# Kernel optimization log

Measured on AMD Instinct MI355X. Metric: run time of the kernel, lower is better.

## Reference

```python
import jax, jax.numpy as jnp
import numpy as np

NUM_HEADS = 16
NUM_T = 8
L1D = 16  # img_size // patch_size


def _freqs_1d(dim, end, base=10000.0):
    f = 1.0 / (base ** (jnp.arange(0, dim, 2, dtype=jnp.float32) / dim))  # [dim/2]
    ang = jnp.outer(jnp.arange(end, dtype=jnp.float32), f)                # [end, dim/2]
    return jnp.cos(ang), jnp.sin(ang)


def _freqs_2d(dim, h, w, base=10000.0):
    f = 1.0 / (base ** (jnp.arange(0, dim, 4, dtype=jnp.float32)[: dim // 4] / dim))  # [dim/4]
    ax = jnp.outer(jnp.arange(w, dtype=jnp.float32), f)  # [w, dim/4]
    ay = jnp.outer(jnp.arange(h, dtype=jnp.float32), f)  # [h, dim/4]
    # flatten order: position index = y*w + x
    ang_x = jnp.broadcast_to(ax[None, :, :], (h, w, dim // 4)).reshape(h * w, dim // 4)
    ang_y = jnp.broadcast_to(ay[:, None, :], (h, w, dim // 4)).reshape(h * w, dim // 4)
    ang = jnp.concatenate([ang_x, ang_y], axis=-1)  # [h*w, dim/2]
    return jnp.cos(ang), jnp.sin(ang)


def _rope(x, cos, sin):
    # x: [..., P, d]; cos/sin: [P, d/2]; interleaved complex pairs (x0,x1),(x2,x3),...
    xr, xi = x[..., 0::2], x[..., 1::2]
    or_ = xr * cos - xi * sin
    oi = xr * sin + xi * cos
    return jnp.stack([or_, oi], axis=-1).reshape(x.shape)


def setup_inputs() -> dict:
    key = jax.random.key(0)
    ks = jax.random.split(key, 5)
    H = 1024
    return {
        "x": jax.random.normal(ks[0], (2, 2048, H), dtype=jnp.float32),
        "w_qkv": jax.random.normal(ks[1], (3 * H, H), dtype=jnp.float32) * 0.02,
        "b_qkv": jax.random.normal(ks[2], (3 * H,), dtype=jnp.float32) * 0.02,
        "w_out": jax.random.normal(ks[3], (H, H), dtype=jnp.float32) * 0.02,
        "b_out": jax.random.normal(ks[4], (H,), dtype=jnp.float32) * 0.02,
    }


def reference(x, w_qkv, b_qkv, w_out, b_out):
    B, L, H = x.shape
    n, t = NUM_HEADS, NUM_T
    hd = H // n
    Ls = L // t  # spatial tokens per frame (= L1D*L1D)

    # QKV projection; per-head layout [q|k|v] of size 3*hd (matches torch rearrange+chunk)
    qkv = (x @ w_qkv.T + b_qkv).reshape(B, L, n, 3 * hd)
    q, k, v = qkv[..., :hd], qkv[..., hd:2 * hd], qkv[..., 2 * hd:]

    cos_s, sin_s = _freqs_2d(hd, L1D, L1D)  # [Ls, hd/2]
    cos_t, sin_t = _freqs_1d(hd, t)         # [t, hd/2]

    def to_bntl(a):  # (B, L=t*Ls, n, hd) -> (B, n, t, Ls, hd)
        return a.reshape(B, t, Ls, n, hd).transpose(0, 3, 1, 2, 4)

    q = _rope(to_bntl(q), cos_s, sin_s)
    k = _rope(to_bntl(k), cos_s, sin_s)
    # temporal rope: rotate over t axis
    q = _rope(q.transpose(0, 1, 3, 2, 4), cos_t, sin_t).transpose(0, 1, 3, 2, 4)
    k = _rope(k.transpose(0, 1, 3, 2, 4), cos_t, sin_t).transpose(0, 1, 3, 2, 4)
    q = q.reshape(B, n, L, hd)
    k = k.reshape(B, n, L, hd)
    v = v.transpose(0, 2, 1, 3)  # (B, n, L, hd)

    scores = jnp.einsum('bnqd,bnkd->bnqk', q, k) / jnp.sqrt(jnp.asarray(hd, jnp.float32))
    idx = jnp.arange(L)
    neg = jnp.finfo(jnp.float32).min
    causal = jnp.where(idx[None, :] <= idx[:, None], 0.0, neg)  # [L, L]
    attn = jax.nn.softmax((scores + causal).astype(jnp.float32), axis=-1).astype(x.dtype)

    o = jnp.einsum('bnqk,bnkd->bnqd', attn, v).transpose(0, 2, 1, 3).reshape(B, L, H)
    o = o * jax.nn.sigmoid(o)  # swish
    return o @ w_out.T + b_out
```

## Files before the change

kernel.cpp:

```cpp
#include <hip/hip_runtime.h>
#include <math.h>

#define B_SZ 2
#define L_SEQ 2048
#define H_SZ 1024
#define NH 16
#define HD 64
#define QSCALE 0.18033688011112042f

typedef __attribute__((ext_vector_type(8))) short frag_ab;
typedef __attribute__((ext_vector_type(4))) float frag_cd;
typedef __attribute__((ext_vector_type(8))) unsigned short u16x8;
typedef __attribute__((ext_vector_type(4))) unsigned short u16x4;

__device__ __forceinline__ unsigned short f2bf(float f) {
  unsigned int x = __builtin_bit_cast(unsigned int, f);
  x += 0x7fffu + ((x >> 16) & 1u);
  return (unsigned short)(x >> 16);
}
__device__ __forceinline__ float bf2f(unsigned int u) {
  return __builtin_bit_cast(float, u << 16);
}
__device__ __forceinline__ unsigned int cvt_pk_bf16(float lo, float hi) {
  unsigned int r;
  asm("v_cvt_pk_bf16_f32 %0, %1, %2" : "=v"(r) : "v"(lo), "v"(hi));
  return r;
}
__device__ __forceinline__ void gload16(const void* g, void* l) {
  __builtin_amdgcn_global_load_lds((const __attribute__((address_space(1))) void*)g,
                                   (__attribute__((address_space(3))) void*)l, 16, 0, 0);
}

__device__ __forceinline__ void cvt8(const float* __restrict__ in,
                                     unsigned short* __restrict__ out, int i) {
  float4 a = *(const float4*)&in[i];
  float4 b = *(const float4*)&in[i + 4];
  u16x8 o = {f2bf(a.x), f2bf(a.y), f2bf(a.z), f2bf(a.w),
             f2bf(b.x), f2bf(b.y), f2bf(b.z), f2bf(b.w)};
  *(u16x8*)&out[i] = o;
}

__global__ __launch_bounds__(256) void glue_pre_k(
    const float* __restrict__ x, const float* __restrict__ wq, const float* __restrict__ wo,
    unsigned short* __restrict__ xb, unsigned short* __restrict__ wqb,
    unsigned short* __restrict__ wob, float2* __restrict__ ctab) {
  int bx = blockIdx.x, tid = threadIdx.x;
  if (bx < 256) {
    int idx = bx * 256 + tid;
    int l = idx >> 5, j = idx & 31;
    int ti = l >> 8;
    int s = l & 255;
    float ang_s;
    if (j < 16) ang_s = (float)(s & 15) * powf(10000.f, -(float)j / 16.f);
    else        ang_s = (float)(s >> 4) * powf(10000.f, -(float)(j - 16) / 16.f);
    float ang_t = (float)ti * powf(10000.f, -(float)j / 32.f);
    float a = ang_s + ang_t;
    ctab[idx] = make_float2(cosf(a), sinf(a));
  } else if (bx < 2304) {
    cvt8(x, xb, ((bx - 256) * 256 + tid) * 8);
  } else if (bx < 3840) {
    cvt8(wq, wqb, ((bx - 2304) * 256 + tid) * 8);
  } else {
    cvt8(wo, wob, ((bx - 3840) * 256 + tid) * 8);
  }
}

#define G_ISSUE(k0, bi)                                                        \
  _Pragma("unroll") for (int it = 0; it < 2; ++it) {                           \
    int c = tid + it * 256;                                                    \
    int row = c >> 2, e0 = (c & 3) * 8;                                        \
    gload16(A + (size_t)(m0 + row) * K + (k0) + e0, &As[bi][c * 8]);           \
    gload16(W + (size_t)(n0 + row) * K + (k0) + e0, &Ws[bi][c * 8]);           \
  }

__global__ __launch_bounds__(256) void gemm_qkv_fused_k(
    const unsigned short* __restrict__ A, const unsigned short* __restrict__ W,
    const float* __restrict__ bias, const float2* __restrict__ ctab,
    unsigned short* __restrict__ Qb, unsigned short* __restrict__ Kb,
    unsigned short* __restrict__ Vt) {
  const int K = 1024, N = 3072;
  __shared__ unsigned short As[2][128 * 32];
  __shared__ unsigned short Ws[2][128 * 32];
  const frag_cd fzero = {0.f, 0.f, 0.f, 0.f};
  int tid = threadIdx.x;
  int nbx = N >> 7;
  int nwg = gridDim.x;
  int bid = blockIdx.x;
  int qq = nwg >> 3;
  int bidx = (bid & 7) * qq + (bid >> 3);
  int m0 = (bidx / nbx) * 128, n0 = (bidx % nbx) * 128;
  int w = tid >> 6, lane = tid & 63, t = lane & 15, g = lane >> 4;
  int wm = w >> 1, wn = w & 1;
  frag_cd acc[4][4];
#pragma unroll
  for (int mi = 0; mi < 4; ++mi)
#pragma unroll
    for (int ni = 0; ni < 4; ++ni) acc[mi][ni] = fzero;

  G_ISSUE(0, 0);
  __syncthreads();
  int kb = 0;
  for (int k0 = 0; k0 < K; k0 += 32, kb ^= 1) {
    if (k0 + 32 < K) { G_ISSUE(k0 + 32, kb ^ 1); }
    frag_ab af[4], wf[4];
#pragma unroll
    for (int mi = 0; mi < 4; ++mi)
      af[mi] = *(const frag_ab*)&As[kb][(wm * 64 + mi * 16 + t) * 32 + 8 * g];
#pragma unroll
    for (int ni = 0; ni < 4; ++ni)
      wf[ni] = *(const frag_ab*)&Ws[kb][(wn * 64 + ni * 16 + t) * 32 + 8 * g];
    __builtin_amdgcn_s_setprio(1);
#pragma unroll
    for (int mi = 0; mi < 4; ++mi)
#pragma unroll
      for (int ni = 0; ni < 4; ++ni)
        acc[mi][ni] = __builtin_amdgcn_mfma_f32_16x16x32_bf16(af[mi], wf[ni], acc[mi][ni], 0, 0, 0);
    __builtin_amdgcn_s_setprio(0);
    __syncthreads();
  }

#pragma unroll
  for (int ni = 0; ni < 4; ++ni) {
    int cb = n0 + wn * 64 + ni * 16;
    int region = (cb >> 6) % 3;
    int head = cb / 192;
    int d = (cb & 63) + t;
    float bv = bias[cb + t];
    if (region == 2) {
#pragma unroll
      for (int mi = 0; mi < 4; ++mi) {
        int row0 = m0 + wm * 64 + mi * 16 + g * 4;
        int bb = row0 >> 11, l0 = row0 & 2047;
        u16x4 ov;
#pragma unroll
        for (int r = 0; r < 4; ++r) ov[r] = f2bf(acc[mi][ni][r] + bv);
        *(u16x4*)&Vt[((size_t)((bb * NH + head) * HD + d)) * L_SEQ + l0] = ov;
      }
    } else {
      float qs = (region == 0) ? QSCALE : 1.f;
      float sgn = (t & 1) ? qs : -qs;
      unsigned short* dst = (region == 0) ? Qb : Kb;
      int j = d >> 1;
#pragma unroll
      for (int mi = 0; mi < 4; ++mi) {
        int row0 = m0 + wm * 64 + mi * 16 + g * 4;
        int bb = row0 >> 11, l0 = row0 & 2047;
        size_t obase = ((size_t)(bb * NH + head) * L_SEQ + l0) * HD + d;
#pragma unroll
        for (int r = 0; r < 4; ++r) {
          float v = acc[mi][ni][r] + bv;
          float p = __shfl_xor(v, 1);
          float2 cs = ctab[(l0 + r) * 32 + j];
          float o = v * (cs.x * qs) + p * (cs.y * sgn);
          dst[obase + (size_t)r * HD] = f2bf(o);
        }
      }
    }
  }
}

__global__ __launch_bounds__(256) void gemm_mfma_k(
    const unsigned short* __restrict__ A, const unsigned short* __restrict__ W,
    const float* __restrict__ bias, float* __restrict__ C, int M, int N, int K) {
  __shared__ unsigned short As[2][128 * 32];
  __shared__ unsigned short Ws[2][128 * 32];
  const frag_cd fzero = {0.f, 0.f, 0.f, 0.f};
  int tid = threadIdx.x;
  int nbx = N >> 7;
  int nwg = gridDim.x;
  int bid = blockIdx.x;
  int qq = nwg >> 3;
  int bidx = (bid & 7) * qq + (bid >> 3);
  int m0 = (bidx / nbx) * 128, n0 = (bidx % nbx) * 128;
  int w = tid >> 6, lane = tid & 63, t = lane & 15, g = lane >> 4;
  int wm = w >> 1, wn = w & 1;
  frag_cd acc[4][4];
#pragma unroll
  for (int mi = 0; mi < 4; ++mi)
#pragma unroll
    for (int ni = 0; ni < 4; ++ni) acc[mi][ni] = fzero;

  G_ISSUE(0, 0);
  __syncthreads();
  int kb = 0;
  for (int k0 = 0; k0 < K; k0 += 32, kb ^= 1) {
    if (k0 + 32 < K) { G_ISSUE(k0 + 32, kb ^ 1); }
    frag_ab af[4], wf[4];
#pragma unroll
    for (int mi = 0; mi < 4; ++mi)
      af[mi] = *(const frag_ab*)&As[kb][(wm * 64 + mi * 16 + t) * 32 + 8 * g];
#pragma unroll
    for (int ni = 0; ni < 4; ++ni)
      wf[ni] = *(const frag_ab*)&Ws[kb][(wn * 64 + ni * 16 + t) * 32 + 8 * g];
    __builtin_amdgcn_s_setprio(1);
#pragma unroll
    for (int mi = 0; mi < 4; ++mi)
#pragma unroll
      for (int ni = 0; ni < 4; ++ni)
        acc[mi][ni] = __builtin_amdgcn_mfma_f32_16x16x32_bf16(af[mi], wf[ni], acc[mi][ni], 0, 0, 0);
    __builtin_amdgcn_s_setprio(0);
    __syncthreads();
  }
#pragma unroll
  for (int mi = 0; mi < 4; ++mi)
#pragma unroll
    for (int ni = 0; ni < 4; ++ni) {
      int col = n0 + wn * 64 + ni * 16 + t;
      float bv = bias[col];
#pragma unroll
      for (int r = 0; r < 4; ++r)
        C[(size_t)(m0 + wm * 64 + mi * 16 + g * 4 + r) * N + col] = acc[mi][ni][r] + bv;
    }
}

__device__ __forceinline__ void attn_tile(
    const unsigned short* __restrict__ Ksb, const unsigned short* __restrict__ Vsb,
    unsigned short* __restrict__ pw,
    const frag_ab* qf, frag_cd* oacc, float& l_run,
    int qrow, bool diag, int kt, int t, int g) {
  const frag_cd cinit = {-32.f, -32.f, -32.f, -32.f};
  frag_cd st[4];
  __builtin_amdgcn_s_setprio(1);
#pragma unroll
  for (int kb = 0; kb < 4; ++kb) {
    frag_ab k0f = *(const frag_ab*)&Ksb[(((kb * 16 + t) * 64) + 8 * g) ^ ((t & 7) << 3)];
    frag_ab k1f = *(const frag_ab*)&Ksb[(((kb * 16 + t) * 64) + 32 + 8 * g) ^ ((t & 7) << 3)];
    st[kb] = __builtin_amdgcn_mfma_f32_16x16x32_bf16(k0f, qf[0], cinit, 0, 0, 0);
    st[kb] = __builtin_amdgcn_mfma_f32_16x16x32_bf16(k1f, qf[1], st[kb], 0, 0, 0);
  }
  __builtin_amdgcn_s_setprio(0);
  float sv[16];
#pragma unroll
  for (int kb = 0; kb < 4; ++kb)
#pragma unroll
    for (int r = 0; r < 4; ++r) {
      float x = st[kb][r];
      if (diag && (kt * 64 + kb * 16 + g * 4 + r) > qrow) x = -1e30f;
      sv[kb * 4 + r] = x;
    }
  float psum = 0.f;
  unsigned int pk[8];
#pragma unroll
  for (int i = 0; i < 8; ++i) {
    float p0 = __builtin_amdgcn_exp2f(sv[2 * i]);
    float p1 = __builtin_amdgcn_exp2f(sv[2 * i + 1]);
    psum += p0 + p1;
    pk[i] = cvt_pk_bf16(p0, p1);
  }
  psum += __shfl_xor(psum, 16);
  psum += __shfl_xor(psum, 32);
  l_run += psum;

#pragma unroll
  for (int kb = 0; kb < 4; ++kb) {
    uint2 pr = {pk[kb * 2], pk[kb * 2 + 1]};
    *(uint2*)&pw[(t * 64 + kb * 16 + g * 4) ^ ((t & 7) << 3)] = pr;
  }
  frag_ab pf0 = *(const frag_ab*)&pw[(t * 64 + 8 * g) ^ ((t & 7) << 3)];
  frag_ab pf1 = *(const frag_ab*)&pw[(t * 64 + 32 + 8 * g) ^ ((t & 7) << 3)];
  const frag_cd fzero = {0.f, 0.f, 0.f, 0.f};
  (void)fzero;
  __builtin_amdgcn_s_setprio(1);
#pragma unroll
  for (int db = 0; db < 4; ++db) {
    frag_ab v0f = *(const frag_ab*)&Vsb[(((db * 16 + t) * 64) + 8 * g) ^ ((t & 7) << 3)];
    frag_ab v1f = *(const frag_ab*)&Vsb[(((db * 16 + t) * 64) + 32 + 8 * g) ^ ((t & 7) << 3)];
    oacc[db] = __builtin_amdgcn_mfma_f32_16x16x32_bf16(v0f, pf0, oacc[db], 0, 0, 0);
    oacc[db] = __builtin_amdgcn_mfma_f32_16x16x32_bf16(v1f, pf1, oacc[db], 0, 0, 0);
  }
  __builtin_amdgcn_s_setprio(0);
}

__global__ __launch_bounds__(512) void attn_mfma_k(
    const unsigned short* __restrict__ Qg, const unsigned short* __restrict__ Kg,
    const unsigned short* __restrict__ Vt, unsigned short* __restrict__ Og) {
  __shared__ unsigned short Ks[2][64 * 64];
  __shared__ unsigned short Vs[2][64 * 64];
  __shared__ unsigned short Ps[8][16 * 64];
  const frag_cd fzero = {0.f, 0.f, 0.f, 0.f};
  int bx = blockIdx.x;
  int qtA = bx & 15;
  int n = (bx >> 4) & 15;
  int b = bx >> 8;
  int qtB = 31 - qtA;
  int tid = threadIdx.x;
  int w = tid >> 6, lane = tid & 63, t = lane & 15, g = lane >> 4;
  int side = w >> 2;
  int qt = side ? qtA : qtB;
  size_t kvbase = ((size_t)(b * NH + n)) * L_SEQ * HD;
  int qrow = qt * 64 + (w & 3) * 16 + t;

  const unsigned short* qp = Qg + kvbase + (size_t)qrow * HD;
  frag_ab qf[2] = {*(const frag_ab*)(qp + 8 * g), *(const frag_ab*)(qp + 32 + 8 * g)};

  frag_cd oacc[4];
#pragma unroll
  for (int db = 0; db < 4; ++db) oacc[db] = fzero;
  float l_run = 0.f;

  int srow = tid >> 3, se0 = (tid & 7) * 8;
  int sdst = (srow * 64 + se0) ^ ((srow & 7) << 3);
  u16x8 kreg = *(const u16x8*)(Kg + kvbase + (size_t)srow * HD + se0);
  u16x8 vreg = *(const u16x8*)(Vt + kvbase + (size_t)srow * L_SEQ + se0);
  *(u16x8*)&Ks[0][sdst] = kreg;
  *(u16x8*)&Vs[0][sdst] = vreg;

  for (int kt = 0; kt <= qtB; ++kt) {
    int cur = kt & 1;
    __syncthreads();
    if (kt < qtB) {
      kreg = *(const u16x8*)(Kg + kvbase + (size_t)((kt + 1) * 64 + srow) * HD + se0);
      vreg = *(const u16x8*)(Vt + kvbase + (size_t)srow * L_SEQ + (kt + 1) * 64 + se0);
    }
    if (kt <= qt)
      attn_tile(&Ks[cur][0], &Vs[cur][0], &Ps[w][0], qf, oacc, l_run, qrow,
                kt == qt, kt, t, g);
    if (kt < qtB) {
      int nxt = cur ^ 1;
      *(u16x8*)&Ks[nxt][sdst] = kreg;
      *(u16x8*)&Vs[nxt][sdst] = vreg;
    }
  }

  size_t ob0 = (size_t)b * L_SEQ * H_SZ + n * 64;
  float inv = 1.f / l_run;
#pragma unroll
  for (int db = 0; db < 4; ++db) {
    u16x4 ov;
#pragma unroll
    for (int r = 0; r < 4; ++r) {
      float o = oacc[db][r] * inv;
      o = o / (1.f + __expf(-o));
      ov[r] = f2bf(o);
    }
    *(u16x4*)&Og[ob0 + (size_t)qrow * H_SZ + db * 16 + g * 4] = ov;
  }
}

extern "C" void kernel_launch(void* const* d_in, const int* in_sizes, int n_in,
                              void* d_out, int out_size, void* d_ws, size_t ws_size,
                              hipStream_t stream) {
  const float* x = (const float*)d_in[0];
  const float* w_qkv = (const float*)d_in[1];
  const float* b_qkv = (const float*)d_in[2];
  const float* w_out = (const float*)d_in[3];
  const float* b_out = (const float*)d_in[4];
  float* out = (float*)d_out;

  float* ws = (float*)d_ws;
  float2* ctab = (float2*)ws;
  unsigned short* us = (unsigned short*)(ws + 131072);
  unsigned short* Qb = us;
  unsigned short* Kb = Qb + 4194304;
  unsigned short* Vt = Kb + 4194304;
  unsigned short* Og = Vt + 4194304;
  unsigned short* xb = Og + 4194304;
  unsigned short* wqkvb = xb + 4194304;
  unsigned short* woutb = wqkvb + 3145728;

  glue_pre_k<<<4352, 256, 0, stream>>>(x, w_qkv, w_out, xb, wqkvb, woutb, ctab);

  gemm_qkv_fused_k<<<768, 256, 0, stream>>>(xb, wqkvb, b_qkv, ctab, Qb, Kb, Vt);

  attn_mfma_k<<<B_SZ * NH * 16, 512, 0, stream>>>(Qb, Kb, Vt, Og);

  gemm_mfma_k<<<256, 256, 0, stream>>>(Og, woutb, b_out, out, 4096, 1024, 1024);
}
```

Before: 113.1 us.

## Transpose rope table and Q layout, halve out-GEMM M tile, defer softmax row sum

The rope cos/sin table is stored j-major, so the QKV epilogue reads four consecutive positions with two vector loads instead of four scattered float2 loads. Q is now written transposed (d-major, like V), so each write is a 4-wide vector store; the attention kernel in turn gathers Q fragments with strided scalar loads. The output projection GEMM uses a 64x128 tile and launches 512 blocks instead of 256, which fills more CUs at the cost of less reuse per block. The softmax denominator is kept per lane and reduced across lanes only once at the end, removing two shuffles per key tile.

```diff
diff --git a/kernel.cpp b/kernel.cpp
--- a/kernel.cpp
+++ b/kernel.cpp
@@ -47,7 +47,7 @@
   int bx = blockIdx.x, tid = threadIdx.x;
   if (bx < 256) {
     int idx = bx * 256 + tid;
-    int l = idx >> 5, j = idx & 31;
+    int j = idx >> 11, l = idx & 2047;
     int ti = l >> 8;
     int s = l & 255;
     float ang_s;
@@ -76,7 +76,7 @@
 __global__ __launch_bounds__(256) void gemm_qkv_fused_k(
     const unsigned short* __restrict__ A, const unsigned short* __restrict__ W,
     const float* __restrict__ bias, const float2* __restrict__ ctab,
-    unsigned short* __restrict__ Qb, unsigned short* __restrict__ Kb,
+    unsigned short* __restrict__ Qt, unsigned short* __restrict__ Kb,
     unsigned short* __restrict__ Vt) {
   const int K = 1024, N = 3072;
   __shared__ unsigned short As[2][128 * 32];
@@ -136,33 +136,57 @@
         for (int r = 0; r < 4; ++r) ov[r] = f2bf(acc[mi][ni][r] + bv);
         *(u16x4*)&Vt[((size_t)((bb * NH + head) * HD + d)) * L_SEQ + l0] = ov;
       }
+    } else if (region == 0) {
+      float sgn = (t & 1) ? QSCALE : -QSCALE;
+      int j = d >> 1;
+#pragma unroll
+      for (int mi = 0; mi < 4; ++mi) {
+        int row0 = m0 + wm * 64 + mi * 16 + g * 4;
+        int bb = row0 >> 11, l0 = row0 & 2047;
+        const float2* cp = ctab + (size_t)j * 2048 + l0;
+        float4 v01 = *(const float4*)cp;
+        float4 v23 = *(const float4*)(cp + 2);
+        float cvec[4] = {v01.x, v01.z, v23.x, v23.z};
+        float svec[4] = {v01.y, v01.w, v23.y, v23.w};
+        u16x4 ov;
+#pragma unroll
+        for (int r = 0; r < 4; ++r) {
+          float v = acc[mi][ni][r] + bv;
+          float p = __shfl_xor(v, 1);
+          float o = v * (cvec[r] * QSCALE) + p * (svec[r] * sgn);
+          ov[r] = f2bf(o);
+        }
+        *(u16x4*)&Qt[((size_t)((bb * NH + head) * HD + d)) * L_SEQ + l0] = ov;
+      }
     } else {
-      float qs = (region == 0) ? QSCALE : 1.f;
-      float sgn = (t & 1) ? qs : -qs;
-      unsigned short* dst = (region == 0) ? Qb : Kb;
+      float sgn = (t & 1) ? 1.f : -1.f;
       int j = d >> 1;
 #pragma unroll
       for (int mi = 0; mi < 4; ++mi) {
         int row0 = m0 + wm * 64 + mi * 16 + g * 4;
         int bb = row0 >> 11, l0 = row0 & 2047;
         size_t obase = ((size_t)(bb * NH + head) * L_SEQ + l0) * HD + d;
+        const float2* cp = ctab + (size_t)j * 2048 + l0;
+        float4 v01 = *(const float4*)cp;
+        float4 v23 = *(const float4*)(cp + 2);
+        float cvec[4] = {v01.x, v01.z, v23.x, v23.z};
+        float svec[4] = {v01.y, v01.w, v23.y, v23.w};
 #pragma unroll
         for (int r = 0; r < 4; ++r) {
           float v = acc[mi][ni][r] + bv;
           float p = __shfl_xor(v, 1);
-          float2 cs = ctab[(l0 + r) * 32 + j];
-          float o = v * (cs.x * qs) + p * (cs.y * sgn);
-          dst[obase + (size_t)r * HD] = f2bf(o);
+          float o = v * cvec[r] + p * (svec[r] * sgn);
+          Kb[obase + (size_t)r * HD] = f2bf(o);
         }
       }
     }
   }
 }
 
-__global__ __launch_bounds__(256) void gemm_mfma_k(
+__global__ __launch_bounds__(256) void gemm_out_k(
     const unsigned short* __restrict__ A, const unsigned short* __restrict__ W,
     const float* __restrict__ bias, float* __restrict__ C, int M, int N, int K) {
-  __shared__ unsigned short As[2][128 * 32];
+  __shared__ unsigned short As[2][64 * 32];
   __shared__ unsigned short Ws[2][128 * 32];
   const frag_cd fzero = {0.f, 0.f, 0.f, 0.f};
   int tid = threadIdx.x;
@@ -171,30 +195,41 @@
   int bid = blockIdx.x;
   int qq = nwg >> 3;
   int bidx = (bid & 7) * qq + (bid >> 3);
-  int m0 = (bidx / nbx) * 128, n0 = (bidx % nbx) * 128;
+  int m0 = (bidx / nbx) * 64, n0 = (bidx % nbx) * 128;
   int w = tid >> 6, lane = tid & 63, t = lane & 15, g = lane >> 4;
   int wm = w >> 1, wn = w & 1;
-  frag_cd acc[4][4];
-#pragma unroll
-  for (int mi = 0; mi < 4; ++mi)
+  frag_cd acc[2][4];
+#pragma unroll
+  for (int mi = 0; mi < 2; ++mi)
 #pragma unroll
     for (int ni = 0; ni < 4; ++ni) acc[mi][ni] = fzero;
 
-  G_ISSUE(0, 0);
+#define G_ISSUE2(k0, bi)                                                       \
+  {                                                                            \
+    int rowA = tid >> 2, e0A = (tid & 3) * 8;                                  \
+    gload16(A + (size_t)(m0 + rowA) * K + (k0) + e0A, &As[bi][tid * 8]);       \
+    _Pragma("unroll") for (int it = 0; it < 2; ++it) {                         \
+      int c = tid + it * 256;                                                  \
+      int row = c >> 2, e0 = (c & 3) * 8;                                      \
+      gload16(W + (size_t)(n0 + row) * K + (k0) + e0, &Ws[bi][c * 8]);         \
+    }                                                                          \
+  }
+
+  G_ISSUE2(0, 0);
   __syncthreads();
   int kb = 0;
   for (int k0 = 0; k0 < K; k0 += 32, kb ^= 1) {
-    if (k0 + 32 < K) { G_ISSUE(k0 + 32, kb ^ 1); }
-    frag_ab af[4], wf[4];
-#pragma unroll
-    for (int mi = 0; mi < 4; ++mi)
-      af[mi] = *(const frag_ab*)&As[kb][(wm * 64 + mi * 16 + t) * 32 + 8 * g];
+    if (k0 + 32 < K) { G_ISSUE2(k0 + 32, kb ^ 1); }
+    frag_ab af[2], wf[4];
+#pragma unroll
+    for (int mi = 0; mi < 2; ++mi)
+      af[mi] = *(const frag_ab*)&As[kb][(wm * 32 + mi * 16 + t) * 32 + 8 * g];
 #pragma unroll
     for (int ni = 0; ni < 4; ++ni)
       wf[ni] = *(const frag_ab*)&Ws[kb][(wn * 64 + ni * 16 + t) * 32 + 8 * g];
     __builtin_amdgcn_s_setprio(1);
 #pragma unroll
-    for (int mi = 0; mi < 4; ++mi)
+    for (int mi = 0; mi < 2; ++mi)
 #pragma unroll
       for (int ni = 0; ni < 4; ++ni)
         acc[mi][ni] = __builtin_amdgcn_mfma_f32_16x16x32_bf16(af[mi], wf[ni], acc[mi][ni], 0, 0, 0);
@@ -202,21 +237,21 @@
     __syncthreads();
   }
 #pragma unroll
-  for (int mi = 0; mi < 4; ++mi)
+  for (int mi = 0; mi < 2; ++mi)
 #pragma unroll
     for (int ni = 0; ni < 4; ++ni) {
       int col = n0 + wn * 64 + ni * 16 + t;
       float bv = bias[col];
 #pragma unroll
       for (int r = 0; r < 4; ++r)
-        C[(size_t)(m0 + wm * 64 + mi * 16 + g * 4 + r) * N + col] = acc[mi][ni][r] + bv;
+        C[(size_t)(m0 + wm * 32 + mi * 16 + g * 4 + r) * N + col] = acc[mi][ni][r] + bv;
     }
 }
 
 __device__ __forceinline__ void attn_tile(
     const unsigned short* __restrict__ Ksb, const unsigned short* __restrict__ Vsb,
     unsigned short* __restrict__ pw,
-    const frag_ab* qf, frag_cd* oacc, float& l_run,
+    const frag_ab* qf, frag_cd* oacc, float& l_part,
     int qrow, bool diag, int kt, int t, int g) {
   const frag_cd cinit = {-32.f, -32.f, -32.f, -32.f};
   frag_cd st[4];
@@ -229,27 +264,20 @@
     st[kb] = __builtin_amdgcn_mfma_f32_16x16x32_bf16(k1f, qf[1], st[kb], 0, 0, 0);
   }
   __builtin_amdgcn_s_setprio(0);
-  float sv[16];
-#pragma unroll
-  for (int kb = 0; kb < 4; ++kb)
-#pragma unroll
-    for (int r = 0; r < 4; ++r) {
-      float x = st[kb][r];
-      if (diag && (kt * 64 + kb * 16 + g * 4 + r) > qrow) x = -1e30f;
-      sv[kb * 4 + r] = x;
-    }
-  float psum = 0.f;
   unsigned int pk[8];
 #pragma unroll
   for (int i = 0; i < 8; ++i) {
-    float p0 = __builtin_amdgcn_exp2f(sv[2 * i]);
-    float p1 = __builtin_amdgcn_exp2f(sv[2 * i + 1]);
-    psum += p0 + p1;
+    int kb = i >> 1, r0 = (2 * i) & 3;
+    float x0 = st[kb][r0], x1 = st[kb][r0 + 1];
+    if (diag) {
+      if ((kt * 64 + kb * 16 + g * 4 + r0) > qrow) x0 = -1e30f;
+      if ((kt * 64 + kb * 16 + g * 4 + r0 + 1) > qrow) x1 = -1e30f;
+    }
+    float p0 = __builtin_amdgcn_exp2f(x0);
+    float p1 = __builtin_amdgcn_exp2f(x1);
+    l_part += p0 + p1;
     pk[i] = cvt_pk_bf16(p0, p1);
   }
-  psum += __shfl_xor(psum, 16);
-  psum += __shfl_xor(psum, 32);
-  l_run += psum;
 
 #pragma unroll
   for (int kb = 0; kb < 4; ++kb) {
@@ -258,8 +286,6 @@
   }
   frag_ab pf0 = *(const frag_ab*)&pw[(t * 64 + 8 * g) ^ ((t & 7) << 3)];
   frag_ab pf1 = *(const frag_ab*)&pw[(t * 64 + 32 + 8 * g) ^ ((t & 7) << 3)];
-  const frag_cd fzero = {0.f, 0.f, 0.f, 0.f};
-  (void)fzero;
   __builtin_amdgcn_s_setprio(1);
 #pragma unroll
   for (int db = 0; db < 4; ++db) {
@@ -272,7 +298,7 @@
 }
 
 __global__ __launch_bounds__(512) void attn_mfma_k(
-    const unsigned short* __restrict__ Qg, const unsigned short* __restrict__ Kg,
+    const unsigned short* __restrict__ Qt, const unsigned short* __restrict__ Kg,
     const unsigned short* __restrict__ Vt, unsigned short* __restrict__ Og) {
   __shared__ unsigned short Ks[2][64 * 64];
   __shared__ unsigned short Vs[2][64 * 64];
@@ -290,13 +316,19 @@
   size_t kvbase = ((size_t)(b * NH + n)) * L_SEQ * HD;
   int qrow = qt * 64 + (w & 3) * 16 + t;
 
-  const unsigned short* qp = Qg + kvbase + (size_t)qrow * HD;
-  frag_ab qf[2] = {*(const frag_ab*)(qp + 8 * g), *(const frag_ab*)(qp + 32 + 8 * g)};
+  const unsigned short* qtp = Qt + kvbase + qrow;
+  frag_ab qf0, qf1;
+#pragma unroll
+  for (int j = 0; j < 8; ++j) {
+    qf0[j] = (short)qtp[(size_t)(8 * g + j) * L_SEQ];
+    qf1[j] = (short)qtp[(size_t)(32 + 8 * g + j) * L_SEQ];
+  }
+  frag_ab qf[2] = {qf0, qf1};
 
   frag_cd oacc[4];
 #pragma unroll
   for (int db = 0; db < 4; ++db) oacc[db] = fzero;
-  float l_run = 0.f;
+  float l_part = 0.f;
 
   int srow = tid >> 3, se0 = (tid & 7) * 8;
   int sdst = (srow * 64 + se0) ^ ((srow & 7) << 3);
@@ -313,7 +345,7 @@
       vreg = *(const u16x8*)(Vt + kvbase + (size_t)srow * L_SEQ + (kt + 1) * 64 + se0);
     }
     if (kt <= qt)
-      attn_tile(&Ks[cur][0], &Vs[cur][0], &Ps[w][0], qf, oacc, l_run, qrow,
+      attn_tile(&Ks[cur][0], &Vs[cur][0], &Ps[w][0], qf, oacc, l_part, qrow,
                 kt == qt, kt, t, g);
     if (kt < qtB) {
       int nxt = cur ^ 1;
@@ -322,6 +354,8 @@
     }
   }
 
+  float l_run = l_part + __shfl_xor(l_part, 16);
+  l_run += __shfl_xor(l_run, 32);
   size_t ob0 = (size_t)b * L_SEQ * H_SZ + n * 64;
   float inv = 1.f / l_run;
 #pragma unroll
@@ -350,8 +384,8 @@
   float* ws = (float*)d_ws;
   float2* ctab = (float2*)ws;
   unsigned short* us = (unsigned short*)(ws + 131072);
-  unsigned short* Qb = us;
-  unsigned short* Kb = Qb + 4194304;
+  unsigned short* Qt = us;
+  unsigned short* Kb = Qt + 4194304;
   unsigned short* Vt = Kb + 4194304;
   unsigned short* Og = Vt + 4194304;
   unsigned short* xb = Og + 4194304;
@@ -360,9 +394,9 @@
 
   glue_pre_k<<<4352, 256, 0, stream>>>(x, w_qkv, w_out, xb, wqkvb, woutb, ctab);
 
-  gemm_qkv_fused_k<<<768, 256, 0, stream>>>(xb, wqkvb, b_qkv, ctab, Qb, Kb, Vt);
-
-  attn_mfma_k<<<B_SZ * NH * 16, 512, 0, stream>>>(Qb, Kb, Vt, Og);
-
-  gemm_mfma_k<<<256, 256, 0, stream>>>(Og, woutb, b_out, out, 4096, 1024, 1024);
-}
+  gemm_qkv_fused_k<<<768, 256, 0, stream>>>(xb, wqkvb, b_qkv, ctab, Qt, Kb, Vt);
+
+  attn_mfma_k<<<B_SZ * NH * 16, 512, 0, stream>>>(Qt, Kb, Vt, Og);
+
+  gemm_out_k<<<512, 256, 0, stream>>>(Og, woutb, b_out, out, 4096, 1024, 1024);
+}
```

Result: slower. 120.4 us (+6.4%).
